# Performance work log

Measured on AMD Instinct MI355X. Metric: run time of the kernel, lower is better.

Reference implementation:

```python
import jax, jax.numpy as jnp
import numpy as np

KH = KW = 3
STRIDE = 1
ITERATIONS = 2
EPS = 1e-7


def _squash(s):
    # squash along last axis (capsule dim)
    sn = jnp.sum(s * s, axis=-1, keepdims=True)
    return (sn / (1.0 + sn)) * s / jnp.sqrt(sn + EPS)


def setup_inputs() -> dict:
    key = jax.random.key(0)
    k1, k2 = jax.random.split(key)
    x = jax.random.normal(k1, (4, 14, 14, 32, 8), dtype=jnp.float32)
    # W: [1,1,1,filters_out, caps_per_patch=3*3*32, dims_out=16, dims_in=8], stddev=0.1 init
    W = 0.1 * jax.random.normal(k2, (1, 1, 1, 32, 288, 16, 8), dtype=jnp.float32)
    return {"x": x, "W": W}


def reference(x, W):
    B, H, Wd, Fin, Din = x.shape
    Ho = (H - KH) // STRIDE + 1
    Wo = (Wd - KW) // STRIDE + 1
    # Patch extraction, channel order (kh, kw, Fin) to match tf.image.extract_patches
    patches = jnp.stack(
        [x[:, i:i + Ho * STRIDE:STRIDE, j:j + Wo * STRIDE:STRIDE]
         for i in range(KH) for j in range(KW)],
        axis=3,
    )  # [B,Ho,Wo,KH*KW,Fin,Din]
    patches = patches.reshape(B, Ho, Wo, KH * KW * Fin, Din)  # [B,Ho,Wo,C,Di]

    Wm = W[0, 0, 0]  # [F, C, Do, Di]
    F, C, Do, _ = Wm.shape
    # predictions[b,h,w,f,c,o] = sum_i W[f,c,o,i] * patches[b,h,w,c,i]
    preds = jnp.einsum('fcoi,bhwci->bhwfco', Wm, patches)

    logits = jnp.zeros((B, Ho, Wo, F, C), dtype=preds.dtype)
    outputs = jnp.zeros((B, Ho, Wo, F, Do), dtype=preds.dtype)
    for _ in range(ITERATIONS):
        # agreement = predictions^T @ outputs over the dims_out axis
        agreement = jnp.einsum('bhwfco,bhwfo->bhwfc', preds, outputs)
        logits = logits + agreement
        # NOTE: original code softmaxes over axis=3 (the filters_out axis)
        cc = jax.nn.softmax(logits, axis=3)  # [B,Ho,Wo,F,C]
        centroids = jnp.sum(cc[..., None] * preds, axis=4)  # [B,Ho,Wo,F,Do]
        outputs = _squash(centroids)
    return outputs
```

## Files before the change

kernel.cpp:

```cpp
#include <hip/hip_runtime.h>

#define NB   4
#define H_IN 14
#define W_IN 14
#define FIN  32
#define DI   8
#define F    32
#define C    288
#define DO   16
#define HO   12
#define WO   12
#define NPOS (NB*HO*WO)
#define EPS  1e-7f

#define CH   16
#define CC   (C/CH)
#define GP   4
#define GRID (CH*(NPOS/GP))

#define KTOT (C*DI)
#define KPAD 2312

#define W2H_BYTES  ((size_t)F*C*DO*DI*2)
#define WH_BYTES   ((size_t)F*C*DO*DI*2)
#define PH_BYTES   ((size_t)NPOS*KTOT*2)
#define PART_BYTES ((size_t)CH*NPOS*F*DO*4)
#define OUT1_BYTES ((size_t)NPOS*F*DO*4)

#define CVT_W2H 576
#define CVT_WH  576
#define CVT_PH  648
#define CVT_GRID (CVT_W2H + CVT_WH + CVT_PH)

typedef _Float16 h2 __attribute__((ext_vector_type(2)));
typedef _Float16 h8v __attribute__((ext_vector_type(8)));
typedef float    f4v __attribute__((ext_vector_type(4)));

__device__ __forceinline__ unsigned int pack2(float a, float b) {
    h2 v; v.x = (_Float16)a; v.y = (_Float16)b;
    return __builtin_bit_cast(unsigned int, v);
}

__device__ __forceinline__ float dot8h(const uint4 w, const uint4 v, float acc) {
#if __has_builtin(__builtin_amdgcn_fdot2)
    acc = __builtin_amdgcn_fdot2(__builtin_bit_cast(h2, w.x), __builtin_bit_cast(h2, v.x), acc, false);
    acc = __builtin_amdgcn_fdot2(__builtin_bit_cast(h2, w.y), __builtin_bit_cast(h2, v.y), acc, false);
    acc = __builtin_amdgcn_fdot2(__builtin_bit_cast(h2, w.z), __builtin_bit_cast(h2, v.z), acc, false);
    acc = __builtin_amdgcn_fdot2(__builtin_bit_cast(h2, w.w), __builtin_bit_cast(h2, v.w), acc, false);
#else
    const h2 w0 = __builtin_bit_cast(h2, w.x), v0 = __builtin_bit_cast(h2, v.x);
    const h2 w1 = __builtin_bit_cast(h2, w.y), v1 = __builtin_bit_cast(h2, v.y);
    const h2 w2 = __builtin_bit_cast(h2, w.z), v2 = __builtin_bit_cast(h2, v.z);
    const h2 w3 = __builtin_bit_cast(h2, w.w), v3 = __builtin_bit_cast(h2, v.w);
    acc += (float)w0.x*(float)v0.x + (float)w0.y*(float)v0.y
         + (float)w1.x*(float)v1.x + (float)w1.y*(float)v1.y
         + (float)w2.x*(float)v2.x + (float)w2.y*(float)v2.y
         + (float)w3.x*(float)v3.x + (float)w3.y*(float)v3.y;
#endif
    return acc;
}

__device__ __forceinline__ int xbase_of(int pos) {
    const int b = pos/(HO*WO), rem = pos%(HO*WO), ho = rem/WO, wo = rem%WO;
    return ((b*H_IN + ho)*W_IN + wo)*FIN*DI;
}

__device__ __forceinline__ int coff_of(int c) {
    const int slab = c >> 5, fin = c & 31;
    const int kh = slab/3, kw = slab%3;
    return (kh*W_IN + kw)*FIN*DI + fin*DI;
}

__global__ __launch_bounds__(256) void kernConv(const float* __restrict__ Wt,
                                                const float* __restrict__ x,
                                                unsigned short* __restrict__ W2h,
                                                unsigned short* __restrict__ Wh,
                                                unsigned short* __restrict__ Ph) {
    const int b = blockIdx.x;
    if (b < CVT_W2H) {
        const int idx = b*256 + threadIdx.x;
        const float* src = Wt + (size_t)idx*8;
        const float4 a = *(const float4*)src;
        const float4 bb = *(const float4*)(src + 4);
        uint4 r;
        r.x = pack2(a.x, a.y);   r.y = pack2(a.z, a.w);
        r.z = pack2(bb.x, bb.y); r.w = pack2(bb.z, bb.w);
        const int o = idx & 15;
        const int c = (idx >> 4) % C;
        const int f = idx / (C*DO);
        ((uint4*)W2h)[(size_t)(c*DO + o)*F + f] = r;
    } else if (b < CVT_W2H + CVT_WH) {
        const int idx = (b - CVT_W2H)*256 + threadIdx.x;
        const float* src = Wt + (size_t)idx*8;
        const float4 a = *(const float4*)src;
        const float4 bb = *(const float4*)(src + 4);
        uint4 r;
        r.x = pack2(a.x, a.y);   r.y = pack2(a.z, a.w);
        r.z = pack2(bb.x, bb.y); r.w = pack2(bb.z, bb.w);
        ((uint4*)Wh)[idx] = r;
    } else {
        const int pc = (b - CVT_W2H - CVT_WH)*256 + threadIdx.x;
        const int pos = pc / C, c = pc % C;
        const float* src = x + xbase_of(pos) + coff_of(c);
        const float4 a = *(const float4*)src;
        const float4 bb = *(const float4*)(src + 4);
        uint4 r;
        r.x = pack2(a.x, a.y);   r.y = pack2(a.z, a.w);
        r.z = pack2(bb.x, bb.y); r.w = pack2(bb.z, bb.w);
        ((uint4*)Ph)[pc] = r;
    }
}

__global__ __launch_bounds__(512) void kernM1(const unsigned short* __restrict__ Ph,
                                              const unsigned short* __restrict__ Wh,
                                              float* __restrict__ out1)
{
    __shared__ unsigned short As[16][KPAD];
    __shared__ f4v red2[4][64];

    const int tid  = threadIdx.x;
    const int lane = tid & 63;
    const int wv   = tid >> 6;
    const int pt   = blockIdx.x >> 3;
    const int fg   = blockIdx.x & 7;
    const int f    = (wv & 3)*8 + fg;
    const int ks   = wv >> 2;
    const int pos0 = pt*16;
    const int n    = lane & 15, q = lane >> 4;

    #pragma unroll
    for (int r = 0; r < 9; ++r) {
        const int linear = r*512 + tid;
        const int row = linear / 288, col8 = linear % 288;
        const uint4 v = *(const uint4*)(Ph + (size_t)(pos0 + row)*KTOT + col8*8);
        *(uint4*)&As[row][col8*8] = v;
    }
    __syncthreads();

    const unsigned short* pa = &As[n][q*8];
    const unsigned short* pb = Wh + ((size_t)(f*C + q)*DO + n)*DI;

    f4v acc0 = {0.f,0.f,0.f,0.f}, acc1 = {0.f,0.f,0.f,0.f};
    const int s0 = ks*36;
    #pragma unroll 4
    for (int s = s0; s < s0 + 36; s += 2) {
        const h8v a0 = *(const h8v*)(pa + s*32);
        const h8v b0 = *(const h8v*)(pb + (size_t)s*4*DO*DI);
        const h8v a1 = *(const h8v*)(pa + (s+1)*32);
        const h8v b1 = *(const h8v*)(pb + (size_t)(s+1)*4*DO*DI);
        acc0 = __builtin_amdgcn_mfma_f32_16x16x32_f16(a0, b0, acc0, 0, 0, 0);
        acc1 = __builtin_amdgcn_mfma_f32_16x16x32_f16(a1, b1, acc1, 0, 0, 0);
    }

    f4v tot;
    #pragma unroll
    for (int r = 0; r < 4; ++r) tot[r] = acc0[r] + acc1[r];

    if (wv >= 4) red2[wv - 4][lane] = tot;
    __syncthreads();

    if (wv < 4) {
        const f4v other = red2[wv][lane];
        #pragma unroll
        for (int r = 0; r < 4; ++r) {
            const float v = (tot[r] + other[r]) * (1.f/32.f);
            float sq = v*v;
            sq += __shfl_xor(sq, 1);
            sq += __shfl_xor(sq, 2);
            sq += __shfl_xor(sq, 4);
            sq += __shfl_xor(sq, 8);
            const float sc = (sq/(1.f + sq)) * rsqrtf(sq + EPS);
            out1[(size_t)(pos0 + q*4 + r)*512 + f*DO + n] = v * sc;
        }
    }
}

__global__ __launch_bounds__(256) void kern2n(const unsigned short* __restrict__ Ph,
                                              const unsigned short* __restrict__ W2h,
                                              const float* __restrict__ out1,
                                              float* __restrict__ part2)
{
    __shared__ float red[2][4][GP][32];
    __shared__ float ccs[2][GP][32];

    const int tid = threadIdx.x;
    const int f  = tid & 31;
    const int og = tid >> 5;
    const int o0 = 2*og, o1 = o0 + 1;
    const int wv = tid >> 6;
    const int half = (tid >> 5) & 1;
    const int ch = blockIdx.x & (CH-1);
    const int pg = blockIdx.x >> 4;

    int poff[GP];
    #pragma unroll
    for (int p = 0; p < GP; ++p) poff[p] = (pg*GP + p)*KTOT;

    float u0[GP], u1[GP];
    #pragma unroll
    for (int p = 0; p < GP; ++p) {
        const float* up = out1 + (size_t)(pg*GP + p)*512 + f*DO;
        u0[p] = up[o0];
        u1[p] = up[o1];
    }

    const uint4* W2h4 = (const uint4*)W2h;
    const int c0 = ch*CC;

    float acc0[GP], acc1[GP];
    #pragma unroll
    for (int p = 0; p < GP; ++p) { acc0[p] = 0.f; acc1[p] = 0.f; }

    #pragma unroll 1
    for (int cl = 0; cl < CC; ++cl) {
        const int c = c0 + cl;
        const int buf = cl & 1;
        const uint4 w0 = W2h4[(size_t)(c*DO + o0)*F + f];
        const uint4 w1 = W2h4[(size_t)(c*DO + o1)*F + f];

        float pred0[GP], pred1[GP];
        #pragma unroll
        for (int p = 0; p < GP; ++p) {
            const uint4 xv = *(const uint4*)(Ph + poff[p] + c*DI);
            pred0[p] = dot8h(w0, xv, 0.f);
            pred1[p] = dot8h(w1, xv, 0.f);
        }

        #pragma unroll
        for (int p = 0; p < GP; ++p) {
            float ap = pred0[p]*u0[p] + pred1[p]*u1[p];
            ap += __shfl_xor(ap, 32);
            if (half == 0) red[buf][wv][p][f] = ap;
        }
        __syncthreads();

        if (tid < GP*32) {
            const int p2 = tid >> 5, f2 = tid & 31;
            const float agr = red[buf][0][p2][f2] + red[buf][1][p2][f2]
                            + red[buf][2][p2][f2] + red[buf][3][p2][f2];
            float m = agr;
            m = fmaxf(m, __shfl_xor(m, 1));
            m = fmaxf(m, __shfl_xor(m, 2));
            m = fmaxf(m, __shfl_xor(m, 4));
            m = fmaxf(m, __shfl_xor(m, 8));
            m = fmaxf(m, __shfl_xor(m, 16));
            const float e = __expf(agr - m);
            float s = e;
            s += __shfl_xor(s, 1);
            s += __shfl_xor(s, 2);
            s += __shfl_xor(s, 4);
            s += __shfl_xor(s, 8);
            s += __shfl_xor(s, 16);
            ccs[buf][p2][f2] = e / s;
        }
        __syncthreads();

        #pragma unroll
        for (int p = 0; p < GP; ++p) {
            const float cv = ccs[buf][p][f];
            acc0[p] += cv*pred0[p];
            acc1[p] += cv*pred1[p];
        }
    }

    #pragma unroll
    for (int p = 0; p < GP; ++p) {
        const size_t base = ((size_t)(ch*NPOS + pg*GP + p))*DO;
        part2[(base + o0)*F + f] = acc0[p];
        part2[(base + o1)*F + f] = acc1[p];
    }
}

__global__ __launch_bounds__(256) void kern3(const float* __restrict__ part2,
                                             float* __restrict__ out)
{
    const int tid = threadIdx.x;
    const int f = tid & 31, p = tid >> 5;
    const int pos = blockIdx.x*8 + p;

    float cent[DO];
    #pragma unroll
    for (int o = 0; o < DO; ++o) cent[o] = 0.f;
    #pragma unroll 1
    for (int k = 0; k < CH; ++k) {
        const float* s = part2 + (size_t)(k*NPOS + pos)*512 + f;
        #pragma unroll
        for (int o = 0; o < DO; ++o) cent[o] += s[o*F];
    }
    float sn = 0.f;
    #pragma unroll
    for (int o = 0; o < DO; ++o) sn += cent[o]*cent[o];
    const float sc = (sn/(1.f + sn)) * rsqrtf(sn + EPS);
    float* dst = out + ((size_t)pos*F + f)*DO;
    #pragma unroll
    for (int o = 0; o < DO; ++o) dst[o] = cent[o]*sc;
}

__device__ __forceinline__ float dot8(const float4* __restrict__ w,
                                      const float4 p0, const float4 p1) {
    float4 a = w[0], b = w[1];
    return a.x*p0.x + a.y*p0.y + a.z*p0.z + a.w*p0.w
         + b.x*p1.x + b.y*p1.y + b.z*p1.z + b.w*p1.w;
}

__global__ __launch_bounds__(256) void capsule_kernel_f32(
    const float* __restrict__ x, const float* __restrict__ Wt,
    float* __restrict__ out)
{
    __shared__ float patch[C*DI];
    __shared__ float cent[F*DO];
    __shared__ float out1[F*DO];
    __shared__ float agr[F*C];
    __shared__ float scale_s[F];

    const int tid = threadIdx.x;
    const int pos = blockIdx.x;
    const int b   = pos / (HO*WO);
    const int rem = pos % (HO*WO);
    const int ho  = rem / WO;
    const int wo  = rem % WO;

    #pragma unroll
    for (int slab = 0; slab < 9; ++slab) {
        const int kh = slab / 3, kw = slab % 3;
        const float* src = x + (((b*H_IN + ho + kh)*W_IN + (wo + kw))*FIN)*DI;
        patch[slab*256 + tid] = src[tid];
    }
    __syncthreads();

    const float4* pv = (const float4*)patch;

    {
        const int fo0 = tid, fo1 = tid + 256;
        const int f0 = fo0 >> 4, o0 = fo0 & 15;
        const int f1 = fo1 >> 4, o1 = fo1 & 15;
        float acc0 = 0.f, acc1 = 0.f;
        for (int c = 0; c < C; ++c) {
            const float4 p0 = pv[c*2], p1 = pv[c*2+1];
            acc0 += dot8((const float4*)(Wt + ((f0*C + c)*DO + o0)*DI), p0, p1);
            acc1 += dot8((const float4*)(Wt + ((f1*C + c)*DO + o1)*DI), p0, p1);
        }
        cent[fo0] = acc0 * (1.f/32.f);
        cent[fo1] = acc1 * (1.f/32.f);
    }
    __syncthreads();

    if (tid < F) {
        float sn = 0.f;
        #pragma unroll
        for (int o = 0; o < DO; ++o) { float v = cent[tid*DO + o]; sn += v*v; }
        const float sc = (sn/(1.f + sn)) * rsqrtf(sn + EPS);
        #pragma unroll
        for (int o = 0; o < DO; ++o) out1[tid*DO + o] = cent[tid*DO + o] * sc;
    }
    __syncthreads();

    #pragma unroll 1
    for (int r = 0; r < (F*C)/256; ++r) {
        const int pp = tid + 256*r;
        const int f = pp / C, c = pp % C;
        const float4* wrow = (const float4*)(Wt + (f*C + c)*DO*DI);
        const float4 p0 = pv[c*2], p1 = pv[c*2+1];
        float a = 0.f;
        #pragma unroll
        for (int o = 0; o < DO; ++o) a += dot8(wrow + o*2, p0, p1) * out1[f*DO + o];
        agr[pp] = a;
    }
    __syncthreads();

    for (int c = tid; c < C; c += 256) {
        float m = -1e30f;
        #pragma unroll
        for (int f = 0; f < F; ++f) m = fmaxf(m, agr[f*C + c]);
        float s = 0.f;
        #pragma unroll
        for (int f = 0; f < F; ++f) {
            const float e = __expf(agr[f*C + c] - m);
            agr[f*C + c] = e; s += e;
        }
        const float inv = 1.f / s;
        #pragma unroll
        for (int f = 0; f < F; ++f) agr[f*C + c] *= inv;
    }
    __syncthreads();

    {
        const int fo0 = tid, fo1 = tid + 256;
        const int f0 = fo0 >> 4, o0 = fo0 & 15;
        const int f1 = fo1 >> 4, o1 = fo1 & 15;
        float acc0 = 0.f, acc1 = 0.f;
        for (int c = 0; c < C; ++c) {
            const float4 p0 = pv[c*2], p1 = pv[c*2+1];
            acc0 += agr[f0*C + c] * dot8((const float4*)(Wt + ((f0*C + c)*DO + o0)*DI), p0, p1);
            acc1 += agr[f1*C + c] * dot8((const float4*)(Wt + ((f1*C + c)*DO + o1)*DI), p0, p1);
        }
        cent[fo0] = acc0;
        cent[fo1] = acc1;
    }
    __syncthreads();

    if (tid < F) {
        float sn = 0.f;
        #pragma unroll
        for (int o = 0; o < DO; ++o) { float v = cent[tid*DO + o]; sn += v*v; }
        scale_s[tid] = (sn/(1.f + sn)) * rsqrtf(sn + EPS);
    }
    __syncthreads();

    out[pos*(F*DO) + tid]       = cent[tid]       * scale_s[tid >> 4];
    out[pos*(F*DO) + tid + 256] = cent[tid + 256] * scale_s[(tid >> 4) + 16];
}

extern "C" void kernel_launch(void* const* d_in, const int* in_sizes, int n_in,
                              void* d_out, int out_size, void* d_ws, size_t ws_size,
                              hipStream_t stream) {
    const float* x  = (const float*)d_in[0];
    const float* Wt = (const float*)d_in[1];
    float* out = (float*)d_out;

    if (ws_size >= W2H_BYTES + WH_BYTES + PH_BYTES + PART_BYTES + OUT1_BYTES) {
        char* p = (char*)d_ws;
        unsigned short* W2h = (unsigned short*)p;            p += W2H_BYTES;
        unsigned short* Wh  = (unsigned short*)p;            p += WH_BYTES;
        unsigned short* Ph  = (unsigned short*)p;            p += PH_BYTES;
        float* part = (float*)p;                             p += PART_BYTES;
        float* out1 = (float*)p;

        kernConv<<<CVT_GRID, 256, 0, stream>>>(Wt, x, W2h, Wh, Ph);
        kernM1<<<36*8, 512, 0, stream>>>(Ph, Wh, out1);
        kern2n<<<GRID, 256, 0, stream>>>(Ph, W2h, out1, part);
        kern3<<<NPOS/8, 256, 0, stream>>>(part, out);
    } else {
        capsule_kernel_f32<<<NPOS, 256, 0, stream>>>(x, Wt, out);
    }
}
```

Before: 131.6 us.

## Remap routing kernel so one wavefront owns a position group, removing block barriers

Kernel 2 is restructured so each 64-lane wavefront handles a whole group of four positions, with each lane covering 8 output dims instead of 2. The agreement reduction and softmax over filters now finish inside the wavefront with shuffles, which drops the shared-memory staging and the two __syncthreads per capsule iteration. In exchange each thread holds more registers (8x4 preds, accumulators and u values) and the grid has a quarter as many blocks, which may lower occupancy.

New measurement: 140.9 us. 1.07x slower.

```diff
diff --git a/kernel.cpp b/kernel.cpp
--- a/kernel.cpp
+++ b/kernel.cpp
@@ -16,7 +16,8 @@
 #define CH   16
 #define CC   (C/CH)
 #define GP   4
-#define GRID (CH*(NPOS/GP))
+#define NGRP (NPOS/GP)
+#define GRID2 ((CH*NGRP)/4)
 
 #define KTOT (C*DI)
 #define KPAD 2312
@@ -175,99 +176,92 @@
     }
 }
 
-__global__ __launch_bounds__(256) void kern2n(const unsigned short* __restrict__ Ph,
+__global__ __launch_bounds__(256) void kern2w(const unsigned short* __restrict__ Ph,
                                               const unsigned short* __restrict__ W2h,
                                               const float* __restrict__ out1,
                                               float* __restrict__ part2)
 {
-    __shared__ float red[2][4][GP][32];
-    __shared__ float ccs[2][GP][32];
-
-    const int tid = threadIdx.x;
-    const int f  = tid & 31;
-    const int og = tid >> 5;
-    const int o0 = 2*og, o1 = o0 + 1;
-    const int wv = tid >> 6;
-    const int half = (tid >> 5) & 1;
-    const int ch = blockIdx.x & (CH-1);
-    const int pg = blockIdx.x >> 4;
-
-    int poff[GP];
-    #pragma unroll
-    for (int p = 0; p < GP; ++p) poff[p] = (pg*GP + p)*KTOT;
-
-    float u0[GP], u1[GP];
+    const int tid  = threadIdx.x;
+    const int lane = tid & 63;
+    const int wv   = tid >> 6;
+    const int f    = lane & 31;
+    const int og   = lane >> 5;
+    const int o0   = og*8;
+
+    const int ch   = blockIdx.x & (CH-1);
+    const int gq   = blockIdx.x >> 4;
+    const int grp  = __builtin_amdgcn_readfirstlane(gq*4 + wv);
+    const int pos0 = grp*GP;
+
+    const int c0 = ch*CC;
+    const uint4* W2h4 = (const uint4*)W2h;
+
+    float u[8][GP];
     #pragma unroll
     for (int p = 0; p < GP; ++p) {
-        const float* up = out1 + (size_t)(pg*GP + p)*512 + f*DO;
-        u0[p] = up[o0];
-        u1[p] = up[o1];
-    }
-
-    const uint4* W2h4 = (const uint4*)W2h;
-    const int c0 = ch*CC;
-
-    float acc0[GP], acc1[GP];
-    #pragma unroll
-    for (int p = 0; p < GP; ++p) { acc0[p] = 0.f; acc1[p] = 0.f; }
+        const float* up = out1 + (size_t)(pos0 + p)*512 + f*DO + o0;
+        const float4 a = *(const float4*)up;
+        const float4 b = *(const float4*)(up + 4);
+        u[0][p]=a.x; u[1][p]=a.y; u[2][p]=a.z; u[3][p]=a.w;
+        u[4][p]=b.x; u[5][p]=b.y; u[6][p]=b.z; u[7][p]=b.w;
+    }
+
+    float acc[8][GP];
+    #pragma unroll
+    for (int k = 0; k < 8; ++k)
+        #pragma unroll
+        for (int p = 0; p < GP; ++p) acc[k][p] = 0.f;
 
     #pragma unroll 1
     for (int cl = 0; cl < CC; ++cl) {
         const int c = c0 + cl;
-        const int buf = cl & 1;
-        const uint4 w0 = W2h4[(size_t)(c*DO + o0)*F + f];
-        const uint4 w1 = W2h4[(size_t)(c*DO + o1)*F + f];
-
-        float pred0[GP], pred1[GP];
+
+        uint4 xv[GP];
+        #pragma unroll
+        for (int p = 0; p < GP; ++p)
+            xv[p] = *(const uint4*)(Ph + (size_t)(pos0 + p)*KTOT + c*DI);
+
+        float pred[8][GP];
+        #pragma unroll
+        for (int k = 0; k < 8; ++k) {
+            const uint4 w = W2h4[(size_t)(c*DO + o0 + k)*F + f];
+            #pragma unroll
+            for (int p = 0; p < GP; ++p) pred[k][p] = dot8h(w, xv[p], 0.f);
+        }
+
         #pragma unroll
         for (int p = 0; p < GP; ++p) {
-            const uint4 xv = *(const uint4*)(Ph + poff[p] + c*DI);
-            pred0[p] = dot8h(w0, xv, 0.f);
-            pred1[p] = dot8h(w1, xv, 0.f);
-        }
-
-        #pragma unroll
-        for (int p = 0; p < GP; ++p) {
-            float ap = pred0[p]*u0[p] + pred1[p]*u1[p];
+            float ap = 0.f;
+            #pragma unroll
+            for (int k = 0; k < 8; ++k) ap += pred[k][p]*u[k][p];
             ap += __shfl_xor(ap, 32);
-            if (half == 0) red[buf][wv][p][f] = ap;
-        }
-        __syncthreads();
-
-        if (tid < GP*32) {
-            const int p2 = tid >> 5, f2 = tid & 31;
-            const float agr = red[buf][0][p2][f2] + red[buf][1][p2][f2]
-                            + red[buf][2][p2][f2] + red[buf][3][p2][f2];
-            float m = agr;
+
+            float m = ap;
             m = fmaxf(m, __shfl_xor(m, 1));
             m = fmaxf(m, __shfl_xor(m, 2));
             m = fmaxf(m, __shfl_xor(m, 4));
             m = fmaxf(m, __shfl_xor(m, 8));
             m = fmaxf(m, __shfl_xor(m, 16));
-            const float e = __expf(agr - m);
+            const float e = __expf(ap - m);
             float s = e;
             s += __shfl_xor(s, 1);
             s += __shfl_xor(s, 2);
             s += __shfl_xor(s, 4);
             s += __shfl_xor(s, 8);
             s += __shfl_xor(s, 16);
-            ccs[buf][p2][f2] = e / s;
-        }
-        __syncthreads();
-
-        #pragma unroll
-        for (int p = 0; p < GP; ++p) {
-            const float cv = ccs[buf][p][f];
-            acc0[p] += cv*pred0[p];
-            acc1[p] += cv*pred1[p];
+            const float cc = e / s;
+
+            #pragma unroll
+            for (int k = 0; k < 8; ++k) acc[k][p] += cc*pred[k][p];
         }
     }
 
     #pragma unroll
     for (int p = 0; p < GP; ++p) {
-        const size_t base = ((size_t)(ch*NPOS + pg*GP + p))*DO;
-        part2[(base + o0)*F + f] = acc0[p];
-        part2[(base + o1)*F + f] = acc1[p];
+        const size_t base = ((size_t)(ch*NPOS + pos0 + p))*DO;
+        #pragma unroll
+        for (int k = 0; k < 8; ++k)
+            part2[(base + o0 + k)*F + f] = acc[k][p];
     }
 }
 
@@ -428,7 +422,7 @@
 
         kernConv<<<CVT_GRID, 256, 0, stream>>>(Wt, x, W2h, Wh, Ph);
         kernM1<<<36*8, 512, 0, stream>>>(Ph, Wh, out1);
-        kern2n<<<GRID, 256, 0, stream>>>(Ph, W2h, out1, part);
+        kern2w<<<GRID2, 256, 0, stream>>>(Ph, W2h, out1, part);
         kern3<<<NPOS/8, 256, 0, stream>>>(part, out);
     } else {
         capsule_kernel_f32<<<NPOS, 256, 0, stream>>>(x, Wt, out);
```
